# Optimization experiments

Hardware: AMD Instinct MI355X
Metric: run time of the kernel (lower is better)

## Reference

```python
import jax, jax.numpy as jnp
import numpy as np

IN_DIM = 256
OUT_DIM = 256


def setup_inputs() -> dict:
    key = jax.random.key(0)
    k1, k2, k3, k4 = jax.random.split(key, 4)
    B, L = 32, 2048
    s_ih = 1.0 / np.sqrt(OUT_DIM)
    x = jax.random.normal(k1, (B, L, IN_DIM), dtype=jnp.float32)
    W_ih = jax.random.uniform(k2, (3 * OUT_DIM, IN_DIM), jnp.float32, -s_ih, s_ih)
    b_ih = jax.random.uniform(k3, (3 * OUT_DIM,), jnp.float32, -s_ih, s_ih)
    W_hh = jax.random.uniform(k4, (3 * OUT_DIM, OUT_DIM), jnp.float32, -s_ih, s_ih)
    return {"x": x, "W_ih": W_ih, "b_ih": b_ih, "W_hh": W_hh}


def reference(x, W_ih, b_ih, W_hh):
    # x: [B, L, D]; W_ih: [3H, D]; b_ih: [3H]; W_hh: [3H, H]
    B, L, _ = x.shape
    H = W_hh.shape[1]
    # Precompute all input-side gate projections in one GEMM: [B, L, 3H]
    xg = jnp.einsum('bld,gd->blg', x, W_ih) + b_ih

    def step(h, xg_t):
        hg = h @ W_hh.T  # [B, 3H]
        # NOTE: module chunks as (update, reset, new) in that order
        x_u, x_r, x_n = jnp.split(xg_t, 3, axis=-1)
        h_u, h_r, h_n = jnp.split(hg, 3, axis=-1)
        r = jax.nn.sigmoid(x_r + h_r)
        z = jax.nn.sigmoid(x_u + h_u)
        n = jnp.tanh(x_n + r * h_n)
        y = z * h + (1.0 - z) * n
        return y, y

    h0 = jnp.zeros((B, H), dtype=x.dtype)
    _, ys = jax.lax.scan(step, h0, jnp.swapaxes(xg, 0, 1))  # ys: [L, B, H]
    return jnp.swapaxes(ys, 0, 1)  # [B, L, H]
```

## Files before the change

kernel.cpp:

```cpp
#include <hip/hip_runtime.h>
#include <hip/hip_bf16.h>
#include <hip/hip_fp16.h>


typedef _Float16 h2v __attribute__((ext_vector_type(2)));
typedef _Float16 h8  __attribute__((ext_vector_type(8)));
typedef __attribute__((ext_vector_type(8))) short s8v;
typedef __attribute__((ext_vector_type(4))) float f4v;

#define PAIR(v, k) __builtin_shufflevector((v), (v), 2 * (k), 2 * (k) + 1)


__device__ __forceinline__ unsigned short f2bf_rne(unsigned u) {
  return (unsigned short)((u + 0x7FFFu + ((u >> 16) & 1u)) >> 16);
}

__global__ void cvt_bf16_k(const float* __restrict__ s, unsigned short* __restrict__ d, int n8) {
  int i = blockIdx.x * blockDim.x + threadIdx.x;
  int st = gridDim.x * blockDim.x;
  const uint4* sp = (const uint4*)s;
  for (; i < n8; i += st) {
    uint4 a = sp[2 * i], b = sp[2 * i + 1];
    union { unsigned short us[8]; uint4 u; } o;
    o.us[0] = f2bf_rne(a.x); o.us[1] = f2bf_rne(a.y);
    o.us[2] = f2bf_rne(a.z); o.us[3] = f2bf_rne(a.w);
    o.us[4] = f2bf_rne(b.x); o.us[5] = f2bf_rne(b.y);
    o.us[6] = f2bf_rne(b.z); o.us[7] = f2bf_rne(b.w);
    ((uint4*)d)[i] = o.u;
  }
}

__global__ void cvt_f16_k(const float* __restrict__ s, __half* __restrict__ d, int n8) {
  int i = blockIdx.x * blockDim.x + threadIdx.x;
  int st = gridDim.x * blockDim.x;
  const float4* sp = (const float4*)s;
  for (; i < n8; i += st) {
    float4 a = sp[2 * i], b = sp[2 * i + 1];
    union { uint4 u; __half2 h[4]; } o;
    o.h[0] = __floats2half2_rn(a.x, a.y);
    o.h[1] = __floats2half2_rn(a.z, a.w);
    o.h[2] = __floats2half2_rn(b.x, b.y);
    o.h[3] = __floats2half2_rn(b.z, b.w);
    ((uint4*)d)[i] = o.u;
  }
}

#define BT 48

__global__ __launch_bounds__(256) void gemm_xg(
    const unsigned short* __restrict__ X, const unsigned short* __restrict__ W,
    const float* __restrict__ bias, __half* __restrict__ XG) {
  __shared__ unsigned short As[128 * BT];
  __shared__ unsigned short Bs[128 * BT];
  const int tid = threadIdx.x;
  const int bm = blockIdx.x, bn = blockIdx.y;
  const int w = tid >> 6, l = tid & 63;
  const int wr = (w >> 1) * 64, wc = (w & 1) * 64;

  f4v acc[4][4];
#pragma unroll
  for (int a = 0; a < 4; ++a)
#pragma unroll
    for (int b = 0; b < 4; ++b) {
      acc[a][b][0] = 0.f; acc[a][b][1] = 0.f; acc[a][b][2] = 0.f; acc[a][b][3] = 0.f;
    }

  const long arow0 = (long)bm * 128;
  const int brow0 = bn * 128;

  for (int kb = 0; kb < 256; kb += 32) {
#pragma unroll
    for (int cc = 0; cc < 2; ++cc) {
      int c = tid + cc * 256;
      int row = c >> 2, part = c & 3;
      uint4 av = *(const uint4*)(X + (arow0 + row) * 256 + kb + part * 8);
      *(uint4*)(&As[row * BT + part * 8]) = av;
      uint4 bv = *(const uint4*)(W + (long)(brow0 + row) * 256 + kb + part * 8);
      *(uint4*)(&Bs[row * BT + part * 8]) = bv;
    }
    __syncthreads();

    const int lr = l & 15, kg = (l >> 4) * 8;
    s8v af[4], bf[4];
#pragma unroll
    for (int mi = 0; mi < 4; ++mi) af[mi] = *(const s8v*)(&As[(wr + mi * 16 + lr) * BT + kg]);
#pragma unroll
    for (int ni = 0; ni < 4; ++ni) bf[ni] = *(const s8v*)(&Bs[(wc + ni * 16 + lr) * BT + kg]);
#pragma unroll
    for (int mi = 0; mi < 4; ++mi)
#pragma unroll
      for (int ni = 0; ni < 4; ++ni)
        acc[mi][ni] = __builtin_amdgcn_mfma_f32_16x16x32_bf16(af[mi], bf[ni], acc[mi][ni], 0, 0, 0);
    __syncthreads();
  }

  const int lr = l & 15, rg = (l >> 4) * 4;
#pragma unroll
  for (int mi = 0; mi < 4; ++mi)
#pragma unroll
    for (int ni = 0; ni < 4; ++ni) {
      int gcol = bn * 128 + wc + ni * 16 + lr;
      float bv = bias[gcol];
#pragma unroll
      for (int r = 0; r < 4; ++r) {
        long grow = arow0 + wr + mi * 16 + rg + r;
        XG[grow * 768 + gcol] = __float2half(acc[mi][ni][r] + bv);
      }
    }
}


__device__ __forceinline__ float fdot2f(h2v a, h2v b, float c) {
#if __has_builtin(__builtin_amdgcn_fdot2)
  return __builtin_amdgcn_fdot2(a, b, c, false);
#else
  return c + (float)a.x * (float)b.x + (float)a.y * (float)b.y;
#endif
}

__device__ __forceinline__ float rcp_fast(float x) {
#if __has_builtin(__builtin_amdgcn_rcpf)
  return __builtin_amdgcn_rcpf(x);
#else
  return 1.f / x;
#endif
}

#define FOR16A(M) M(0) M(1) M(2) M(3) M(4) M(5) M(6) M(7) \
                  M(8) M(9) M(10) M(11) M(12) M(13) M(14) M(15)
#define FOR16B(M) M(16) M(17) M(18) M(19) M(20) M(21) M(22) M(23) \
                  M(24) M(25) M(26) M(27) M(28) M(29) M(30) M(31)

__global__ __launch_bounds__(512)
__attribute__((amdgpu_waves_per_eu(2, 2)))
void gru_rec(
    const __half* __restrict__ Whh, const __half* __restrict__ XG,
    float* __restrict__ Y) {
  const int b = blockIdx.x;
  const int tid = threadIdx.x;
  const int i = tid & 255;
  const int grp = tid >> 8;

  __shared__ __align__(16) __half hl[256];
  __shared__ float r_l[256];
  __shared__ float p1_l[256];

  const uint4* wrow = (const uint4*)(Whh + (long)tid * 256);
  const uint4* wnew = (const uint4*)(Whh + (long)(512 + i) * 256);
  const int rot = grp * 16;

#define DECL_WF(J) h8 wf##J = __builtin_bit_cast(h8, wrow[((J) + rot) & 31]);
#define DECL_UH(J) h8 uh##J = __builtin_bit_cast(h8, wnew[rot + (J)]);
  FOR16A(DECL_WF)
  FOR16B(DECL_WF)
  FOR16A(DECL_UH)
#undef DECL_WF
#undef DECL_UH

  if (grp == 0) hl[i] = __float2half(0.f);
  float h_old = 0.f;
  __syncthreads();

  const long base = (long)b * 2048 * 768;
  const long ybase = (long)b * 2048 * 256;
  const int colA = grp ? (256 + i) : i;

  const uint4* hA = (const uint4*)(&hl[grp * 128]);
  const uint4* hB = (const uint4*)(&hl[(1 - grp) * 128]);

  __half va_c = XG[base + colA];
  __half vb_c = __float2half(0.f);
  if (!grp) vb_c = XG[base + 512 + i];

  for (int t = 0; t < 2048; ++t) {
    const long nx = base + (long)(t + 1 < 2048 ? t + 1 : 2047) * 768;
    __half va_n = XG[nx + colA];
    __half vb_n = vb_c;
    if (!grp) vb_n = XG[nx + 512 + i];

    float a0 = 0.f, a1 = 0.f, b0 = 0.f, b1 = 0.f;

#define DOT_A(J) { h8 hv = __builtin_bit_cast(h8, hA[(J)]);      \
    a0 = fdot2f(PAIR(wf##J, 0), PAIR(hv, 0), a0);                \
    a1 = fdot2f(PAIR(wf##J, 1), PAIR(hv, 1), a1);                \
    a0 = fdot2f(PAIR(wf##J, 2), PAIR(hv, 2), a0);                \
    a1 = fdot2f(PAIR(wf##J, 3), PAIR(hv, 3), a1);                \
    b0 = fdot2f(PAIR(uh##J, 0), PAIR(hv, 0), b0);                \
    b1 = fdot2f(PAIR(uh##J, 1), PAIR(hv, 1), b1);                \
    b0 = fdot2f(PAIR(uh##J, 2), PAIR(hv, 2), b0);                \
    b1 = fdot2f(PAIR(uh##J, 3), PAIR(hv, 3), b1); }
#define DOT_B(J) { h8 hv = __builtin_bit_cast(h8, hB[(J) - 16]); \
    a0 = fdot2f(PAIR(wf##J, 0), PAIR(hv, 0), a0);                \
    a1 = fdot2f(PAIR(wf##J, 1), PAIR(hv, 1), a1);                \
    a0 = fdot2f(PAIR(wf##J, 2), PAIR(hv, 2), a0);                \
    a1 = fdot2f(PAIR(wf##J, 3), PAIR(hv, 3), a1); }

    FOR16A(DOT_A)
    FOR16B(DOT_B)
#undef DOT_A
#undef DOT_B

    const float dF = a0 + a1;
    const float dH = b0 + b1;
    const float xv = __half2float(va_c);

    if (grp) {
      float r = rcp_fast(1.f + __expf(-(xv + dF)));
      r_l[i] = r;
      p1_l[i] = dH;
    }
    __syncthreads();
    if (!grp) {
      float z = rcp_fast(1.f + __expf(-(xv + dF)));
      float hn = dH + p1_l[i];
      float pre = __half2float(vb_c) + r_l[i] * hn;
      float e = __expf(2.f * pre);
      float n = 1.f - 2.f * rcp_fast(1.f + e);
      float hnew = z * h_old + (1.f - z) * n;
      Y[ybase + (long)t * 256 + i] = hnew;
      hl[i] = __float2half(hnew);
      h_old = hnew;
    }
    __syncthreads();
    va_c = va_n;
    vb_c = vb_n;
  }
}


extern "C" void kernel_launch(void* const* d_in, const int* in_sizes, int n_in,
                              void* d_out, int out_size, void* d_ws, size_t ws_size,
                              hipStream_t stream) {
  const float* x   = (const float*)d_in[0];
  const float* Wih = (const float*)d_in[1];
  const float* bih = (const float*)d_in[2];
  const float* Whh = (const float*)d_in[3];
  float* Y = (float*)d_out;

  char* ws = (char*)d_ws;
  unsigned short* x16   = (unsigned short*)ws;
  unsigned short* wih16 = (unsigned short*)(ws + 33554432);
  __half*         whh16 = (__half*)(ws + 33554432 + 393216);
  __half*         xg16  = (__half*)(ws + 33554432 + 2 * 393216);

  cvt_bf16_k<<<2048, 256, 0, stream>>>(x, x16, 16777216 / 8);
  cvt_bf16_k<<<96, 256, 0, stream>>>(Wih, wih16, 196608 / 8);
  cvt_f16_k<<<96, 256, 0, stream>>>(Whh, whh16, 196608 / 8);

  dim3 g(512, 6);
  gemm_xg<<<g, 256, 0, stream>>>(x16, wih16, bih, xg16);

  gru_rec<<<32, 512, 0, stream>>>(whh16, xg16, Y);
}
```

Measured before the change: 2.646 ms.

## Broadcast hidden state via readlane into SGPRs instead of per-lane LDS vector reads

Each wave now loads the 256-element fp16 hidden state once as a uint2 per lane, then extracts each pair with v_readlane into scalar registers for the dot products. This replaces 32 per-lane 16-byte LDS broadcast reads per step. The weight rotation is replaced by grp-dependent branches that pick which chunks carry the new-gate weights. The waves-per-EU hint is relaxed to (1,2), which allows more registers but may change the occupancy plan. It adds 128 readlane instructions per step, and those compete with the VALU dot instructions.

```diff
diff --git a/kernel.cpp b/kernel.cpp
--- a/kernel.cpp
+++ b/kernel.cpp
@@ -130,9 +130,34 @@
                   M(8) M(9) M(10) M(11) M(12) M(13) M(14) M(15)
 #define FOR16B(M) M(16) M(17) M(18) M(19) M(20) M(21) M(22) M(23) \
                   M(24) M(25) M(26) M(27) M(28) M(29) M(30) M(31)
+#define FOR16C(M) M(16,0) M(17,1) M(18,2) M(19,3) M(20,4) M(21,5) M(22,6) M(23,7) \
+                  M(24,8) M(25,9) M(26,10) M(27,11) M(28,12) M(29,13) M(30,14) M(31,15)
+
+#define RLCHUNK(J) \
+  unsigned hpa_##J, hpb_##J, hpc_##J, hpd_##J; \
+  asm("v_readlane_b32 %0, %1, %2" : "=s"(hpa_##J) : "v"(hd.x), "i"(2 * (J))); \
+  asm("v_readlane_b32 %0, %1, %2" : "=s"(hpb_##J) : "v"(hd.y), "i"(2 * (J))); \
+  asm("v_readlane_b32 %0, %1, %2" : "=s"(hpc_##J) : "v"(hd.x), "i"(2 * (J) + 1)); \
+  asm("v_readlane_b32 %0, %1, %2" : "=s"(hpd_##J) : "v"(hd.y), "i"(2 * (J) + 1));
+
+#define DOTF(J) \
+  a0 = fdot2f(__builtin_bit_cast(h2v, hpa_##J), PAIR(wf##J, 0), a0); \
+  a1 = fdot2f(__builtin_bit_cast(h2v, hpb_##J), PAIR(wf##J, 1), a1); \
+  a0 = fdot2f(__builtin_bit_cast(h2v, hpc_##J), PAIR(wf##J, 2), a0); \
+  a1 = fdot2f(__builtin_bit_cast(h2v, hpd_##J), PAIR(wf##J, 3), a1);
+
+#define DOTN(J, U) \
+  b0 = fdot2f(__builtin_bit_cast(h2v, hpa_##J), PAIR(uh##U, 0), b0); \
+  b1 = fdot2f(__builtin_bit_cast(h2v, hpb_##J), PAIR(uh##U, 1), b1); \
+  b0 = fdot2f(__builtin_bit_cast(h2v, hpc_##J), PAIR(uh##U, 2), b0); \
+  b1 = fdot2f(__builtin_bit_cast(h2v, hpd_##J), PAIR(uh##U, 3), b1);
+
+#define CHF(J)     RLCHUNK(J) DOTF(J)
+#define CHN(J)     RLCHUNK(J) DOTF(J) DOTN(J, J)
+#define CHN2(J, U) RLCHUNK(J) DOTF(J) DOTN(J, U)
 
 __global__ __launch_bounds__(512)
-__attribute__((amdgpu_waves_per_eu(2, 2)))
+__attribute__((amdgpu_waves_per_eu(1, 2)))
 void gru_rec(
     const __half* __restrict__ Whh, const __half* __restrict__ XG,
     float* __restrict__ Y) {
@@ -140,17 +165,17 @@
   const int tid = threadIdx.x;
   const int i = tid & 255;
   const int grp = tid >> 8;
+  const int lane = tid & 63;
 
   __shared__ __align__(16) __half hl[256];
   __shared__ float r_l[256];
   __shared__ float p1_l[256];
 
   const uint4* wrow = (const uint4*)(Whh + (long)tid * 256);
-  const uint4* wnew = (const uint4*)(Whh + (long)(512 + i) * 256);
-  const int rot = grp * 16;
-
-#define DECL_WF(J) h8 wf##J = __builtin_bit_cast(h8, wrow[((J) + rot) & 31]);
-#define DECL_UH(J) h8 uh##J = __builtin_bit_cast(h8, wnew[rot + (J)]);
+  const uint4* wnew = (const uint4*)(Whh + (long)(512 + i) * 256 + grp * 128);
+
+#define DECL_WF(J) h8 wf##J = __builtin_bit_cast(h8, wrow[(J)]);
+#define DECL_UH(J) h8 uh##J = __builtin_bit_cast(h8, wnew[(J)]);
   FOR16A(DECL_WF)
   FOR16B(DECL_WF)
   FOR16A(DECL_UH)
@@ -165,9 +190,6 @@
   const long ybase = (long)b * 2048 * 256;
   const int colA = grp ? (256 + i) : i;
 
-  const uint4* hA = (const uint4*)(&hl[grp * 128]);
-  const uint4* hB = (const uint4*)(&hl[(1 - grp) * 128]);
-
   __half va_c = XG[base + colA];
   __half vb_c = __float2half(0.f);
   if (!grp) vb_c = XG[base + 512 + i];
@@ -178,27 +200,16 @@
     __half vb_n = vb_c;
     if (!grp) vb_n = XG[nx + 512 + i];
 
+    uint2 hd = *(const uint2*)(&hl[lane * 4]);
+
     float a0 = 0.f, a1 = 0.f, b0 = 0.f, b1 = 0.f;
-
-#define DOT_A(J) { h8 hv = __builtin_bit_cast(h8, hA[(J)]);      \
-    a0 = fdot2f(PAIR(wf##J, 0), PAIR(hv, 0), a0);                \
-    a1 = fdot2f(PAIR(wf##J, 1), PAIR(hv, 1), a1);                \
-    a0 = fdot2f(PAIR(wf##J, 2), PAIR(hv, 2), a0);                \
-    a1 = fdot2f(PAIR(wf##J, 3), PAIR(hv, 3), a1);                \
-    b0 = fdot2f(PAIR(uh##J, 0), PAIR(hv, 0), b0);                \
-    b1 = fdot2f(PAIR(uh##J, 1), PAIR(hv, 1), b1);                \
-    b0 = fdot2f(PAIR(uh##J, 2), PAIR(hv, 2), b0);                \
-    b1 = fdot2f(PAIR(uh##J, 3), PAIR(hv, 3), b1); }
-#define DOT_B(J) { h8 hv = __builtin_bit_cast(h8, hB[(J) - 16]); \
-    a0 = fdot2f(PAIR(wf##J, 0), PAIR(hv, 0), a0);                \
-    a1 = fdot2f(PAIR(wf##J, 1), PAIR(hv, 1), a1);                \
-    a0 = fdot2f(PAIR(wf##J, 2), PAIR(hv, 2), a0);                \
-    a1 = fdot2f(PAIR(wf##J, 3), PAIR(hv, 3), a1); }
-
-    FOR16A(DOT_A)
-    FOR16B(DOT_B)
-#undef DOT_A
-#undef DOT_B
+    if (!grp) {
+      FOR16A(CHN)
+      FOR16B(CHF)
+    } else {
+      FOR16A(CHF)
+      FOR16C(CHN2)
+    }
 
     const float dF = a0 + a1;
     const float dH = b0 + b1;
```

New measurement: 3.314 ms. +25.2%, slower.

## Split recurrent matvec across lane quads with DPP reduction and double-buffered h

Applied to the files above, without the earlier changes.

Rewrites the recurrent kernel to use 256 threads instead of 512. Each lane quad shares 12 weight rows, and each lane holds one quarter of the K dimension in registers. Partial dot products are combined with a two-step DPP quad reduction, and each thread computes one output's full gate math. The hidden state is double-buffered in shared memory, so each step needs one barrier instead of two, and the r/p1 shared-memory exchange between thread groups goes away. The cost is register pressure from 96 h8 weight registers, per-step DPP and select overhead, and loss of the prefetch of the next step's XG values.

```diff
diff --git a/kernel.cpp b/kernel.cpp
--- a/kernel.cpp
+++ b/kernel.cpp
@@ -126,104 +126,114 @@
 #endif
 }
 
-#define FOR16A(M) M(0) M(1) M(2) M(3) M(4) M(5) M(6) M(7) \
-                  M(8) M(9) M(10) M(11) M(12) M(13) M(14) M(15)
-#define FOR16B(M) M(16) M(17) M(18) M(19) M(20) M(21) M(22) M(23) \
-                  M(24) M(25) M(26) M(27) M(28) M(29) M(30) M(31)
-
-__global__ __launch_bounds__(512)
-__attribute__((amdgpu_waves_per_eu(2, 2)))
+__device__ __forceinline__ float quad_red(float v) {
+  int s1 = __builtin_amdgcn_update_dpp(0, __builtin_bit_cast(int, v),
+                                       0xB1 , 0xF, 0xF, true);
+  float v1 = v + __builtin_bit_cast(float, s1);
+  int s2 = __builtin_amdgcn_update_dpp(0, __builtin_bit_cast(int, v1),
+                                       0x4E , 0xF, 0xF, true);
+  return v1 + __builtin_bit_cast(float, s2);
+}
+
+__device__ __forceinline__ float sel4(int p, float a, float b, float c, float d) {
+  float lo = (p & 1) ? b : a;
+  float hi = (p & 1) ? d : c;
+  return (p & 2) ? hi : lo;
+}
+
+#define FOR12(M) M(0) M(1) M(2) M(3) M(4) M(5) M(6) M(7) M(8) M(9) M(10) M(11)
+
+#define LOADROW(m) \
+  h8 w##m##_0, w##m##_1, w##m##_2, w##m##_3, w##m##_4, w##m##_5, w##m##_6, w##m##_7; \
+  { const uint4* pr_ = (const uint4*)(Whh + (long)(256 * ((m) >> 2) + rs + 64 * ((m) & 3)) * 256 + kq * 64); \
+    w##m##_0 = __builtin_bit_cast(h8, pr_[0]); \
+    w##m##_1 = __builtin_bit_cast(h8, pr_[1]); \
+    w##m##_2 = __builtin_bit_cast(h8, pr_[2]); \
+    w##m##_3 = __builtin_bit_cast(h8, pr_[3]); \
+    w##m##_4 = __builtin_bit_cast(h8, pr_[4]); \
+    w##m##_5 = __builtin_bit_cast(h8, pr_[5]); \
+    w##m##_6 = __builtin_bit_cast(h8, pr_[6]); \
+    w##m##_7 = __builtin_bit_cast(h8, pr_[7]); }
+
+#define PINROW(m) \
+  asm volatile("" : "+v"(w##m##_0), "+v"(w##m##_1), "+v"(w##m##_2), "+v"(w##m##_3), \
+                    "+v"(w##m##_4), "+v"(w##m##_5), "+v"(w##m##_6), "+v"(w##m##_7));
+
+#define DACC(m) float acc##m = 0.f;
+
+#define DCH(m, c) \
+  acc##m = fdot2f(PAIR(w##m##_##c, 0), PAIR(hq##c, 0), acc##m); \
+  acc##m = fdot2f(PAIR(w##m##_##c, 1), PAIR(hq##c, 1), acc##m); \
+  acc##m = fdot2f(PAIR(w##m##_##c, 2), PAIR(hq##c, 2), acc##m); \
+  acc##m = fdot2f(PAIR(w##m##_##c, 3), PAIR(hq##c, 3), acc##m);
+
+#define ROWDOT(m) DCH(m,0) DCH(m,1) DCH(m,2) DCH(m,3) DCH(m,4) DCH(m,5) DCH(m,6) DCH(m,7)
+
+#define DRED(m) float rr##m = quad_red(acc##m);
+
+__global__ __launch_bounds__(256)
+__attribute__((amdgpu_waves_per_eu(1, 1)))
 void gru_rec(
     const __half* __restrict__ Whh, const __half* __restrict__ XG,
     float* __restrict__ Y) {
   const int b = blockIdx.x;
   const int tid = threadIdx.x;
-  const int i = tid & 255;
-  const int grp = tid >> 8;
-
-  __shared__ __align__(16) __half hl[256];
-  __shared__ float r_l[256];
-  __shared__ float p1_l[256];
-
-  const uint4* wrow = (const uint4*)(Whh + (long)tid * 256);
-  const uint4* wnew = (const uint4*)(Whh + (long)(512 + i) * 256);
-  const int rot = grp * 16;
-
-#define DECL_WF(J) h8 wf##J = __builtin_bit_cast(h8, wrow[((J) + rot) & 31]);
-#define DECL_UH(J) h8 uh##J = __builtin_bit_cast(h8, wnew[rot + (J)]);
-  FOR16A(DECL_WF)
-  FOR16B(DECL_WF)
-  FOR16A(DECL_UH)
-#undef DECL_WF
-#undef DECL_UH
-
-  if (grp == 0) hl[i] = __float2half(0.f);
+  const int kq = tid & 3;
+  const int rs = tid >> 2;
+  const int j = rs + 64 * kq;
+
+  __shared__ __align__(16) __half hl[2][256];
+
+  FOR12(LOADROW)
+  FOR12(PINROW)
+
+  hl[0][j] = __float2half(0.f);
   float h_old = 0.f;
   __syncthreads();
 
-  const long base = (long)b * 2048 * 768;
-  const long ybase = (long)b * 2048 * 256;
-  const int colA = grp ? (256 + i) : i;
-
-  const uint4* hA = (const uint4*)(&hl[grp * 128]);
-  const uint4* hB = (const uint4*)(&hl[(1 - grp) * 128]);
-
-  __half va_c = XG[base + colA];
-  __half vb_c = __float2half(0.f);
-  if (!grp) vb_c = XG[base + 512 + i];
+  const unsigned short* xp = (const unsigned short*)XG + (long)b * 2048 * 768 + j;
+  float* yp = Y + (long)b * 2048 * 256 + j;
 
   for (int t = 0; t < 2048; ++t) {
-    const long nx = base + (long)(t + 1 < 2048 ? t + 1 : 2047) * 768;
-    __half va_n = XG[nx + colA];
-    __half vb_n = vb_c;
-    if (!grp) vb_n = XG[nx + 512 + i];
-
-    float a0 = 0.f, a1 = 0.f, b0 = 0.f, b1 = 0.f;
-
-#define DOT_A(J) { h8 hv = __builtin_bit_cast(h8, hA[(J)]);      \
-    a0 = fdot2f(PAIR(wf##J, 0), PAIR(hv, 0), a0);                \
-    a1 = fdot2f(PAIR(wf##J, 1), PAIR(hv, 1), a1);                \
-    a0 = fdot2f(PAIR(wf##J, 2), PAIR(hv, 2), a0);                \
-    a1 = fdot2f(PAIR(wf##J, 3), PAIR(hv, 3), a1);                \
-    b0 = fdot2f(PAIR(uh##J, 0), PAIR(hv, 0), b0);                \
-    b1 = fdot2f(PAIR(uh##J, 1), PAIR(hv, 1), b1);                \
-    b0 = fdot2f(PAIR(uh##J, 2), PAIR(hv, 2), b0);                \
-    b1 = fdot2f(PAIR(uh##J, 3), PAIR(hv, 3), b1); }
-#define DOT_B(J) { h8 hv = __builtin_bit_cast(h8, hB[(J) - 16]); \
-    a0 = fdot2f(PAIR(wf##J, 0), PAIR(hv, 0), a0);                \
-    a1 = fdot2f(PAIR(wf##J, 1), PAIR(hv, 1), a1);                \
-    a0 = fdot2f(PAIR(wf##J, 2), PAIR(hv, 2), a0);                \
-    a1 = fdot2f(PAIR(wf##J, 3), PAIR(hv, 3), a1); }
-
-    FOR16A(DOT_A)
-    FOR16B(DOT_B)
-#undef DOT_A
-#undef DOT_B
-
-    const float dF = a0 + a1;
-    const float dH = b0 + b1;
-    const float xv = __half2float(va_c);
-
-    if (grp) {
-      float r = rcp_fast(1.f + __expf(-(xv + dF)));
-      r_l[i] = r;
-      p1_l[i] = dH;
-    }
+    unsigned short xu_r = xp[0];
+    unsigned short xr_r = xp[256];
+    unsigned short xn_r = xp[512];
+
+    const uint4* hb = (const uint4*)(&hl[t & 1][kq * 64]);
+    h8 hq0 = __builtin_bit_cast(h8, hb[0]);
+    h8 hq1 = __builtin_bit_cast(h8, hb[1]);
+    h8 hq2 = __builtin_bit_cast(h8, hb[2]);
+    h8 hq3 = __builtin_bit_cast(h8, hb[3]);
+    h8 hq4 = __builtin_bit_cast(h8, hb[4]);
+    h8 hq5 = __builtin_bit_cast(h8, hb[5]);
+    h8 hq6 = __builtin_bit_cast(h8, hb[6]);
+    h8 hq7 = __builtin_bit_cast(h8, hb[7]);
+
+    FOR12(DACC)
+    FOR12(ROWDOT)
+    FOR12(DRED)
+
+    const float su = sel4(kq, rr0, rr1, rr2, rr3);
+    const float sr = sel4(kq, rr4, rr5, rr6, rr7);
+    const float sn = sel4(kq, rr8, rr9, rr10, rr11);
+
+    const float xu = __half2float(__builtin_bit_cast(__half, xu_r));
+    const float xr = __half2float(__builtin_bit_cast(__half, xr_r));
+    const float xn = __half2float(__builtin_bit_cast(__half, xn_r));
+
+    float z = rcp_fast(1.f + __expf(-(xu + su)));
+    float r = rcp_fast(1.f + __expf(-(xr + sr)));
+    float pre = xn + r * sn;
+    float e = __expf(2.f * pre);
+    float n = 1.f - 2.f * rcp_fast(1.f + e);
+    float hnew = z * h_old + (1.f - z) * n;
+
+    *yp = hnew;
+    hl[(t & 1) ^ 1][j] = __float2half(hnew);
+    h_old = hnew;
+    xp += 768;
+    yp += 256;
     __syncthreads();
-    if (!grp) {
-      float z = rcp_fast(1.f + __expf(-(xv + dF)));
-      float hn = dH + p1_l[i];
-      float pre = __half2float(vb_c) + r_l[i] * hn;
-      float e = __expf(2.f * pre);
-      float n = 1.f - 2.f * rcp_fast(1.f + e);
-      float hnew = z * h_old + (1.f - z) * n;
-      Y[ybase + (long)t * 256 + i] = hnew;
-      hl[i] = __float2half(hnew);
-      h_old = hnew;
-    }
-    __syncthreads();
-    va_c = va_n;
-    vb_c = vb_n;
   }
 }
 
@@ -250,5 +260,5 @@
   dim3 g(512, 6);
   gemm_xg<<<g, 256, 0, stream>>>(x16, wih16, bih, xg16);
 
-  gru_rec<<<32, 512, 0, stream>>>(whh16, xg16, Y);
-}
+  gru_rec<<<32, 256, 0, stream>>>(whh16, xg16, Y);
+}
```

Measured after the change: 4.216 ms. 59.3% more time.
